# Kernel optimization log

Measured on AMD Instinct MI355X. Metric: run time of the kernel, lower is better.

Reference implementation:

```python
import jax, jax.numpy as jnp
import numpy as np
import math

D_MODEL = 1024
N = 64
TAU_MIN = 1e-4

def _next_pow_two(n: int) -> int:
    return 1 << (n - 1).bit_length()

def setup_inputs() -> dict:
    key = jax.random.key(0)
    ks = jax.random.split(key, 6)
    Bb, T = 4, 8192
    half = N // 2
    n = jnp.arange(half, dtype=jnp.float32)
    x = jax.random.normal(ks[0], (Bb, T, D_MODEL), dtype=jnp.float32)
    log_tau = jnp.full((half,), math.log(0.5), dtype=jnp.float32)
    freq = (math.pi * (2 * n + 1) / 2).astype(jnp.float32)  # hippoD init
    Bp = 1.0 + 0.2 * jax.random.normal(ks[1], (half,), dtype=jnp.float32)
    Cp = (1.0 / math.sqrt(half)) * jax.random.normal(ks[2], (half,), dtype=jnp.float32)
    log_dt = jnp.zeros((), dtype=jnp.float32)
    # torch Linear weight layout: (out_features, in_features)
    W_in = jax.random.normal(ks[3], (half, D_MODEL), dtype=jnp.float32) / math.sqrt(D_MODEL)
    W_out = jax.random.normal(ks[4], (D_MODEL, half), dtype=jnp.float32) / math.sqrt(half)
    return {"x": x, "log_tau": log_tau, "freq": freq, "Bp": Bp, "Cp": Cp,
            "log_dt": log_dt, "W_in": W_in, "W_out": W_out}

def reference(x, log_tau, freq, Bp, Cp, log_dt, W_in, W_out):
    Bb, T, _ = x.shape
    L = _next_pow_two(2 * T)  # static
    half = log_tau.shape[0]
    # ---- analytic kernel (N, T) ----
    dt = jnp.exp(log_dt)
    tau = jnp.clip(jnp.exp(log_tau), TAU_MIN)
    angle = freq * dt                       # (half,)
    log_lam_mag = -tau * dt                 # log of exp(-tau*dt)
    log_gain = jnp.log(jnp.abs(Bp) + 1e-9) + jnp.log(jnp.abs(Cp) + 1e-9)
    i = jnp.arange(T, dtype=x.dtype)
    amp = jnp.exp(log_gain[:, None] + i[None, :] * log_lam_mag[:, None])  # (half, T)
    K_half = amp * jnp.cos(i[None, :] * angle[:, None])                   # (half, T)
    K_full = jnp.concatenate([K_half, K_half[::-1]], axis=0)              # (N, T)
    Kf = jnp.fft.rfft(K_full, n=L, axis=-1)                               # (N, L//2+1)
    # ---- FFT convolution ----
    x_proj = jnp.einsum('btd,nd->btn', x, W_in)                           # (B,T,half)
    x_modes = jnp.concatenate([x_proj, x_proj[..., ::-1]], axis=-1)       # (B,T,N)
    Uf = jnp.fft.rfft(x_modes, n=L, axis=1).transpose(0, 2, 1)            # (B,N,L//2+1)
    Yf = Uf * Kf[None]
    y_modes = jnp.fft.irfft(Yf, n=L, axis=2)[..., :T].transpose(0, 2, 1)  # (B,T,N)
    y = y_modes[..., :half]                                               # (B,T,half)
    return jnp.einsum('btn,dn->btd', y, W_out)
```

## Files before the change

kernel.cpp:

```cpp
#include <hip/hip_runtime.h>
#include <math.h>

#define NB 4
#define TT 8192
#define DM 1024
#define NH 32
#define CT 64
#define NG (TT/CT)
#define DK 128

__global__ __launch_bounds__(256) void k1_proj_scan(
    const float* __restrict__ x, const float* __restrict__ Wi,
    const float* __restrict__ log_tau, const float* __restrict__ freq,
    const float* __restrict__ log_dt,
    float* __restrict__ hl, float* __restrict__ Ech)
{
    __shared__ __align__(16) float xs[CT * 129];
    __shared__ __align__(16) float ws[NH * DK];
    const int c    = blockIdx.x;
    const int b    = blockIdx.y;
    const int t0   = c * CT;
    const int tid  = threadIdx.x;
    const int lane = tid & 63;
    const int ng   = tid >> 6;

    float acc[8] = {0.f, 0.f, 0.f, 0.f, 0.f, 0.f, 0.f, 0.f};
    const float* xb = x + ((size_t)b * TT + t0) * DM;

    for (int dk = 0; dk < DM; dk += DK) {
#pragma unroll
        for (int it = 0; it < 8; ++it) {
            int idx4 = tid + it * 256;
            int tt   = idx4 >> 5;
            int d4   = (idx4 & 31) * 4;
            float4 v = *(const float4*)(xb + (size_t)tt * DM + dk + d4);
            float* p = &xs[tt * 129 + d4];
            p[0] = v.x; p[1] = v.y; p[2] = v.z; p[3] = v.w;
        }
#pragma unroll
        for (int it = 0; it < 4; ++it) {
            int idx4 = tid + it * 256;
            int nn   = idx4 >> 5;
            int d4   = (idx4 & 31) * 4;
            *(float4*)(&ws[nn * DK + d4]) =
                *(const float4*)(Wi + (size_t)nn * DM + dk + d4);
        }
        __syncthreads();
#pragma unroll 2
        for (int d4 = 0; d4 < DK; d4 += 4) {
            const float* xrow = &xs[lane * 129 + d4];
            float x0 = xrow[0], x1 = xrow[1], x2 = xrow[2], x3 = xrow[3];
#pragma unroll
            for (int j = 0; j < 8; ++j) {
                const float4 w = *(const float4*)(&ws[(ng * 8 + j) * DK + d4]);
                acc[j] = fmaf(x3, w.w, fmaf(x2, w.z, fmaf(x1, w.y, fmaf(x0, w.x, acc[j]))));
            }
        }
        __syncthreads();
    }

    const float dtv = expf(log_dt[0]);
    for (int j = 0; j < 8; ++j) {
        const int n = ng * 8 + j;
        const float tau = fmaxf(expf(log_tau[n]), 1e-4f);
        const float rr  = expf(-tau * dtv);
        const float th  = freq[n] * dtv;
        float pr = rr * cosf(th), pi = rr * sinf(th);
        float vr = acc[j], vi = 0.f;
#pragma unroll
        for (int off = 1; off < 64; off <<= 1) {
            float ur = __shfl_up(vr, (unsigned)off);
            float ui = __shfl_up(vi, (unsigned)off);
            if (lane >= off) {
                vr = fmaf(pr, ur, fmaf(-pi, ui, vr));
                vi = fmaf(pr, ui, fmaf( pi, ur, vi));
            }
            float sr = pr * pr - pi * pi;
            float si = 2.f * pr * pi;
            pr = sr; pi = si;
        }
        size_t hb = (((size_t)b * TT + t0 + lane) * NH + n) * 2;
        hl[hb]     = vr;
        hl[hb + 1] = vi;
        if (lane == 63) {
            size_t eb = (((size_t)b * NG + c) * NH + n) * 2;
            Ech[eb]     = vr;
            Ech[eb + 1] = vi;
        }
    }
}

__global__ __launch_bounds__(64) void k2_chunkscan(
    const float* __restrict__ log_tau, const float* __restrict__ freq,
    const float* __restrict__ log_dt,
    const float* __restrict__ Ech, float* __restrict__ Hin)
{
    const int n = threadIdx.x;
    if (n >= NH) return;
    const int c = blockIdx.x;
    const int b = blockIdx.y;
    const double dtv = exp((double)log_dt[0]);
    const double tau = fmax(exp((double)log_tau[n]), 1e-4);
    const double th  = (double)freq[n] * dtv;
    const double m   = exp(-tau * dtv * (double)CT);
    const double a   = th * (double)CT;
    const float Lr = (float)(m * cos(a));
    const float Li = (float)(m * sin(a));
    float hr = 0.f, hi = 0.f;
    for (int cp = 0; cp < c; ++cp) {
        const float* e = Ech + (((size_t)b * NG + cp) * NH + n) * 2;
        float tr = Lr * hr - Li * hi + e[0];
        float ti = Lr * hi + Li * hr + e[1];
        hr = tr; hi = ti;
    }
    float* o = Hin + (((size_t)b * NG + c) * NH + n) * 2;
    o[0] = hr; o[1] = hi;
}

#define ROWFMA(i, s) \
    acc[i].x = fmaf(s, w.x, acc[i].x); acc[i].y = fmaf(s, w.y, acc[i].y); \
    acc[i].z = fmaf(s, w.z, acc[i].z); acc[i].w = fmaf(s, w.w, acc[i].w);

__global__ __launch_bounds__(256) void k3_out(
    const float* __restrict__ hl, const float* __restrict__ Hin,
    const float* __restrict__ Wo,
    const float* __restrict__ log_tau, const float* __restrict__ freq,
    const float* __restrict__ Bp, const float* __restrict__ Cp,
    const float* __restrict__ log_dt,
    float* __restrict__ out)
{
    __shared__ __align__(16) float ysT[NH * 64];
    __shared__ __align__(16) float wT[NH * 260];
    const int c    = blockIdx.x;
    const int b    = blockIdx.y;
    const int t0   = c * CT;
    const int tid  = threadIdx.x;
    const int lane = tid & 63;
    const int ng   = tid >> 6;

    {
        const float dtv = expf(log_dt[0]);
        const int t = lane;
        for (int j = 0; j < 8; ++j) {
            const int n = ng * 8 + j;
            const float tau = fmaxf(expf(log_tau[n]), 1e-4f);
            const float rr  = expf(-tau * dtv);
            const float th  = freq[n] * dtv;
            const float g   = (fabsf(Bp[n]) + 1e-9f) * (fabsf(Cp[n]) + 1e-9f);
            float p2r = rr * cosf(th), p2i = rr * sinf(th);
            float pwr = 1.f, pwi = 0.f;
            const int e = t + 1;
#pragma unroll
            for (int bit = 0; bit < 7; ++bit) {
                if (e & (1 << bit)) {
                    float nr = pwr * p2r - pwi * p2i;
                    float ni = pwr * p2i + pwi * p2r;
                    pwr = nr; pwi = ni;
                }
                float sr = p2r * p2r - p2i * p2i;
                float si = 2.f * p2r * p2i;
                p2r = sr; p2i = si;
            }
            const float* hp = hl  + (((size_t)b * TT + t0 + t) * NH + n) * 2;
            const float* Hp = Hin + (((size_t)b * NG + c) * NH + n) * 2;
            float re = hp[0] + pwr * Hp[0] - pwi * Hp[1];
            ysT[n * 64 + t] = g * re;
        }
    }
    __syncthreads();

    float* const outb = out + ((size_t)b * TT + t0) * DM;
    for (int db = 0; db < DM; db += 256) {
#pragma unroll
        for (int it = 0; it < 32; ++it) {
            int idx = tid + it * 256;
            int dl  = idx >> 5;
            int nn  = idx & 31;
            wT[nn * 260 + dl] = Wo[(size_t)(db + dl) * NH + nn];
        }
        __syncthreads();
        float4 acc[16];
#pragma unroll
        for (int i = 0; i < 16; ++i) acc[i] = make_float4(0.f, 0.f, 0.f, 0.f);
#pragma unroll 4
        for (int n = 0; n < NH; ++n) {
            const float4 w = *(const float4*)(&wT[n * 260 + lane * 4]);
            const float4* yp = (const float4*)(&ysT[n * 64 + ng * 16]);
            const float4 ya = yp[0], yb = yp[1], yc = yp[2], yd = yp[3];
            ROWFMA(0,  ya.x) ROWFMA(1,  ya.y) ROWFMA(2,  ya.z) ROWFMA(3,  ya.w)
            ROWFMA(4,  yb.x) ROWFMA(5,  yb.y) ROWFMA(6,  yb.z) ROWFMA(7,  yb.w)
            ROWFMA(8,  yc.x) ROWFMA(9,  yc.y) ROWFMA(10, yc.z) ROWFMA(11, yc.w)
            ROWFMA(12, yd.x) ROWFMA(13, yd.y) ROWFMA(14, yd.z) ROWFMA(15, yd.w)
        }
#pragma unroll
        for (int i = 0; i < 16; ++i) {
            *(float4*)(outb + (size_t)(ng * 16 + i) * DM + db + lane * 4) = acc[i];
        }
        __syncthreads();
    }
}

extern "C" void kernel_launch(void* const* d_in, const int* in_sizes, int n_in,
                              void* d_out, int out_size, void* d_ws, size_t ws_size,
                              hipStream_t stream)
{
    (void)in_sizes; (void)n_in; (void)out_size; (void)ws_size;
    const float* x       = (const float*)d_in[0];
    const float* log_tau = (const float*)d_in[1];
    const float* freq    = (const float*)d_in[2];
    const float* Bp      = (const float*)d_in[3];
    const float* Cp      = (const float*)d_in[4];
    const float* log_dt  = (const float*)d_in[5];
    const float* Wi      = (const float*)d_in[6];
    const float* Wo      = (const float*)d_in[7];
    float* out = (float*)d_out;

    float* wsf = (float*)d_ws;
    float* hl  = wsf;
    float* Ech = wsf + (size_t)NB * TT * NH * 2;
    float* Hin = Ech + (size_t)NB * NG * NH * 2;

    dim3 grid(NG, NB);
    k1_proj_scan<<<grid, 256, 0, stream>>>(x, Wi, log_tau, freq, log_dt, hl, Ech);
    k2_chunkscan<<<grid, 64, 0, stream>>>(log_tau, freq, log_dt, Ech, Hin);
    k3_out<<<grid, 256, 0, stream>>>(hl, Hin, Wo, log_tau, freq, Bp, Cp, log_dt, out);
}
```

Baseline: 342.5 us.

## Double block size, parallel-scan chunk carries, reorganize hl layout and output tiling

All three kernels are reworked. k1 and k3 move to 512-thread blocks with fewer modes per wave, and k1's shared-memory stores are staggered to cut bank conflicts. k2 replaces the O(NG) sequential carry loop per block with one block per batch that runs a wave-level parallel complex scan over chunk pairs. The intermediate buffers move to a float2 mode-major layout so loads and stores coalesce. k3 tiles its output over 512 columns with scalar strided weight reads, which changes register pressure and the store pattern.

```diff
diff --git a/kernel.cpp b/kernel.cpp
--- a/kernel.cpp
+++ b/kernel.cpp
@@ -8,51 +8,55 @@
 #define CT 64
 #define NG (TT/CT)
 #define DK 128
-
-__global__ __launch_bounds__(256) void k1_proj_scan(
+#define MW 4
+
+__global__ __launch_bounds__(512, 4) void k1_proj_scan(
     const float* __restrict__ x, const float* __restrict__ Wi,
     const float* __restrict__ log_tau, const float* __restrict__ freq,
     const float* __restrict__ log_dt,
-    float* __restrict__ hl, float* __restrict__ Ech)
-{
-    __shared__ __align__(16) float xs[CT * 129];
-    __shared__ __align__(16) float ws[NH * DK];
+    float2* __restrict__ hl, float2* __restrict__ Ech)
+{
+    __shared__ float xs[CT * 129];
+    __shared__ float ws[NH * DK];
     const int c    = blockIdx.x;
     const int b    = blockIdx.y;
     const int t0   = c * CT;
     const int tid  = threadIdx.x;
     const int lane = tid & 63;
-    const int ng   = tid >> 6;
-
-    float acc[8] = {0.f, 0.f, 0.f, 0.f, 0.f, 0.f, 0.f, 0.f};
+    const int wv   = tid >> 6;
+
+    float acc[MW] = {0.f, 0.f, 0.f, 0.f};
     const float* xb = x + ((size_t)b * TT + t0) * DM;
 
     for (int dk = 0; dk < DM; dk += DK) {
 #pragma unroll
-        for (int it = 0; it < 8; ++it) {
-            int idx4 = tid + it * 256;
+        for (int it = 0; it < 4; ++it) {
+            int idx4 = tid + it * 512;
             int tt   = idx4 >> 5;
-            int d4   = (idx4 & 31) * 4;
-            float4 v = *(const float4*)(xb + (size_t)tt * DM + dk + d4);
-            float* p = &xs[tt * 129 + d4];
-            p[0] = v.x; p[1] = v.y; p[2] = v.z; p[3] = v.w;
-        }
-#pragma unroll
-        for (int it = 0; it < 4; ++it) {
-            int idx4 = tid + it * 256;
+            int cc   = idx4 & 31;
+            float4 v = *(const float4*)(xb + (size_t)tt * DM + dk + cc * 4);
+            float vv[4] = {v.x, v.y, v.z, v.w};
+            float* p = &xs[tt * 129 + cc * 4];
+            int q = (idx4 >> 3) & 3;
+#pragma unroll
+            for (int k = 0; k < 4; ++k) { int j = (k + q) & 3; p[j] = vv[j]; }
+        }
+#pragma unroll
+        for (int it = 0; it < 2; ++it) {
+            int idx4 = tid + it * 512;
             int nn   = idx4 >> 5;
             int d4   = (idx4 & 31) * 4;
             *(float4*)(&ws[nn * DK + d4]) =
                 *(const float4*)(Wi + (size_t)nn * DM + dk + d4);
         }
         __syncthreads();
-#pragma unroll 2
+#pragma unroll 4
         for (int d4 = 0; d4 < DK; d4 += 4) {
-            const float* xrow = &xs[lane * 129 + d4];
-            float x0 = xrow[0], x1 = xrow[1], x2 = xrow[2], x3 = xrow[3];
-#pragma unroll
-            for (int j = 0; j < 8; ++j) {
-                const float4 w = *(const float4*)(&ws[(ng * 8 + j) * DK + d4]);
+            const float* xr = &xs[lane * 129 + d4];
+            float x0 = xr[0], x1 = xr[1], x2 = xr[2], x3 = xr[3];
+#pragma unroll
+            for (int j = 0; j < MW; ++j) {
+                const float4 w = *(const float4*)(&ws[(wv * MW + j) * DK + d4]);
                 acc[j] = fmaf(x3, w.w, fmaf(x2, w.z, fmaf(x1, w.y, fmaf(x0, w.x, acc[j]))));
             }
         }
@@ -60,8 +64,9 @@
     }
 
     const float dtv = expf(log_dt[0]);
-    for (int j = 0; j < 8; ++j) {
-        const int n = ng * 8 + j;
+#pragma unroll
+    for (int j = 0; j < MW; ++j) {
+        const int n = wv * MW + j;
         const float tau = fmaxf(expf(log_tau[n]), 1e-4f);
         const float rr  = expf(-tau * dtv);
         const float th  = freq[n] * dtv;
@@ -79,70 +84,81 @@
             float si = 2.f * pr * pi;
             pr = sr; pi = si;
         }
-        size_t hb = (((size_t)b * TT + t0 + lane) * NH + n) * 2;
-        hl[hb]     = vr;
-        hl[hb + 1] = vi;
+        hl[((size_t)(b * NG + c) * NH + n) * CT + lane] = make_float2(vr, vi);
         if (lane == 63) {
-            size_t eb = (((size_t)b * NG + c) * NH + n) * 2;
-            Ech[eb]     = vr;
-            Ech[eb + 1] = vi;
-        }
-    }
-}
-
-__global__ __launch_bounds__(64) void k2_chunkscan(
+            Ech[((size_t)b * NH + n) * NG + c] = make_float2(vr, vi);
+        }
+    }
+}
+
+__global__ __launch_bounds__(256) void k2_chunkscan(
     const float* __restrict__ log_tau, const float* __restrict__ freq,
     const float* __restrict__ log_dt,
-    const float* __restrict__ Ech, float* __restrict__ Hin)
-{
-    const int n = threadIdx.x;
-    if (n >= NH) return;
-    const int c = blockIdx.x;
-    const int b = blockIdx.y;
+    const float2* __restrict__ Ech, float2* __restrict__ Hin)
+{
+    const int b    = blockIdx.x;
+    const int lane = threadIdx.x & 63;
+    const int wv   = threadIdx.x >> 6;
     const double dtv = exp((double)log_dt[0]);
-    const double tau = fmax(exp((double)log_tau[n]), 1e-4);
-    const double th  = (double)freq[n] * dtv;
-    const double m   = exp(-tau * dtv * (double)CT);
-    const double a   = th * (double)CT;
-    const float Lr = (float)(m * cos(a));
-    const float Li = (float)(m * sin(a));
-    float hr = 0.f, hi = 0.f;
-    for (int cp = 0; cp < c; ++cp) {
-        const float* e = Ech + (((size_t)b * NG + cp) * NH + n) * 2;
-        float tr = Lr * hr - Li * hi + e[0];
-        float ti = Lr * hi + Li * hr + e[1];
-        hr = tr; hi = ti;
-    }
-    float* o = Hin + (((size_t)b * NG + c) * NH + n) * 2;
-    o[0] = hr; o[1] = hi;
-}
-
-#define ROWFMA(i, s) \
-    acc[i].x = fmaf(s, w.x, acc[i].x); acc[i].y = fmaf(s, w.y, acc[i].y); \
-    acc[i].z = fmaf(s, w.z, acc[i].z); acc[i].w = fmaf(s, w.w, acc[i].w);
-
-__global__ __launch_bounds__(256) void k3_out(
-    const float* __restrict__ hl, const float* __restrict__ Hin,
+#pragma unroll
+    for (int j = 0; j < 8; ++j) {
+        const int n = wv * 8 + j;
+        const double tau = fmax(exp((double)log_tau[n]), 1e-4);
+        const double a   = (double)freq[n] * dtv * (double)CT;
+        const double m   = exp(-tau * dtv * (double)CT);
+        const float Lr = (float)(m * cos(a));
+        const float Li = (float)(m * sin(a));
+        const float2* eb = Ech + ((size_t)b * NH + n) * NG;
+        float2 e0 = eb[2 * lane];
+        float2 e1 = eb[2 * lane + 1];
+        float vr = fmaf(Lr, e0.x, fmaf(-Li, e0.y, e1.x));
+        float vi = fmaf(Lr, e0.y, fmaf( Li, e0.x, e1.y));
+        float pr = Lr * Lr - Li * Li;
+        float pi = 2.f * Lr * Li;
+#pragma unroll
+        for (int off = 1; off < 64; off <<= 1) {
+            float ur = __shfl_up(vr, (unsigned)off);
+            float ui = __shfl_up(vi, (unsigned)off);
+            if (lane >= off) {
+                vr = fmaf(pr, ur, fmaf(-pi, ui, vr));
+                vi = fmaf(pr, ui, fmaf( pi, ur, vi));
+            }
+            float sr = pr * pr - pi * pi;
+            float si = 2.f * pr * pi;
+            pr = sr; pi = si;
+        }
+        float wr = __shfl_up(vr, 1u), wi = __shfl_up(vi, 1u);
+        if (lane == 0) { wr = 0.f; wi = 0.f; }
+        float2* hb = Hin + ((size_t)b * NH + n) * NG;
+        hb[2 * lane]     = make_float2(wr, wi);
+        hb[2 * lane + 1] = make_float2(fmaf(Lr, wr, fmaf(-Li, wi, e0.x)),
+                                       fmaf(Lr, wi, fmaf( Li, wr, e0.y)));
+    }
+}
+
+__global__ __launch_bounds__(512, 4) void k3_out(
+    const float2* __restrict__ hl, const float2* __restrict__ Hin,
     const float* __restrict__ Wo,
     const float* __restrict__ log_tau, const float* __restrict__ freq,
     const float* __restrict__ Bp, const float* __restrict__ Cp,
     const float* __restrict__ log_dt,
     float* __restrict__ out)
 {
-    __shared__ __align__(16) float ysT[NH * 64];
-    __shared__ __align__(16) float wT[NH * 260];
+    __shared__ float ysT[NH * 64];
+    __shared__ float wT[NH * 513];
     const int c    = blockIdx.x;
     const int b    = blockIdx.y;
     const int t0   = c * CT;
     const int tid  = threadIdx.x;
     const int lane = tid & 63;
-    const int ng   = tid >> 6;
+    const int wv   = tid >> 6;
 
     {
         const float dtv = expf(log_dt[0]);
         const int t = lane;
-        for (int j = 0; j < 8; ++j) {
-            const int n = ng * 8 + j;
+#pragma unroll
+        for (int j = 0; j < 4; ++j) {
+            const int n = wv * 4 + j;
             const float tau = fmaxf(expf(log_tau[n]), 1e-4f);
             const float rr  = expf(-tau * dtv);
             const float th  = freq[n] * dtv;
@@ -161,42 +177,53 @@
                 float si = 2.f * p2r * p2i;
                 p2r = sr; p2i = si;
             }
-            const float* hp = hl  + (((size_t)b * TT + t0 + t) * NH + n) * 2;
-            const float* Hp = Hin + (((size_t)b * NG + c) * NH + n) * 2;
-            float re = hp[0] + pwr * Hp[0] - pwi * Hp[1];
-            ysT[n * 64 + t] = g * re;
-        }
-    }
-    __syncthreads();
-
+            float2 hv = hl[((size_t)(b * NG + c) * NH + n) * CT + t];
+            float2 Hv = Hin[((size_t)b * NH + n) * NG + c];
+            ysT[n * 64 + t] = g * (hv.x + pwr * Hv.x - pwi * Hv.y);
+        }
+    }
+
+    const int qd = wv >> 2;
+    const int tg = wv & 3;
+    const int dbase = qd * 256 + lane;
     float* const outb = out + ((size_t)b * TT + t0) * DM;
-    for (int db = 0; db < DM; db += 256) {
+    for (int db = 0; db < DM; db += 512) {
+        __syncthreads();
 #pragma unroll
         for (int it = 0; it < 32; ++it) {
-            int idx = tid + it * 256;
+            int idx = tid + it * 512;
             int dl  = idx >> 5;
             int nn  = idx & 31;
-            wT[nn * 260 + dl] = Wo[(size_t)(db + dl) * NH + nn];
-        }
-        __syncthreads();
-        float4 acc[16];
-#pragma unroll
-        for (int i = 0; i < 16; ++i) acc[i] = make_float4(0.f, 0.f, 0.f, 0.f);
+            wT[nn * 513 + dl] = Wo[(size_t)(db + dl) * NH + nn];
+        }
+        __syncthreads();
+        float a0[16], a1[16], a2[16], a3[16];
+#pragma unroll
+        for (int i = 0; i < 16; ++i) { a0[i] = a1[i] = a2[i] = a3[i] = 0.f; }
 #pragma unroll 4
         for (int n = 0; n < NH; ++n) {
-            const float4 w = *(const float4*)(&wT[n * 260 + lane * 4]);
-            const float4* yp = (const float4*)(&ysT[n * 64 + ng * 16]);
-            const float4 ya = yp[0], yb = yp[1], yc = yp[2], yd = yp[3];
-            ROWFMA(0,  ya.x) ROWFMA(1,  ya.y) ROWFMA(2,  ya.z) ROWFMA(3,  ya.w)
-            ROWFMA(4,  yb.x) ROWFMA(5,  yb.y) ROWFMA(6,  yb.z) ROWFMA(7,  yb.w)
-            ROWFMA(8,  yc.x) ROWFMA(9,  yc.y) ROWFMA(10, yc.z) ROWFMA(11, yc.w)
-            ROWFMA(12, yd.x) ROWFMA(13, yd.y) ROWFMA(14, yd.z) ROWFMA(15, yd.w)
+            const float w0 = wT[n * 513 + dbase];
+            const float w1 = wT[n * 513 + dbase + 64];
+            const float w2 = wT[n * 513 + dbase + 128];
+            const float w3 = wT[n * 513 + dbase + 192];
+            const float* yr = &ysT[n * 64 + tg * 16];
+#pragma unroll
+            for (int i = 0; i < 16; ++i) {
+                const float yv = yr[i];
+                a0[i] = fmaf(yv, w0, a0[i]);
+                a1[i] = fmaf(yv, w1, a1[i]);
+                a2[i] = fmaf(yv, w2, a2[i]);
+                a3[i] = fmaf(yv, w3, a3[i]);
+            }
         }
 #pragma unroll
         for (int i = 0; i < 16; ++i) {
-            *(float4*)(outb + (size_t)(ng * 16 + i) * DM + db + lane * 4) = acc[i];
-        }
-        __syncthreads();
+            float* op = outb + (size_t)(tg * 16 + i) * DM + db + dbase;
+            op[0]   = a0[i];
+            op[64]  = a1[i];
+            op[128] = a2[i];
+            op[192] = a3[i];
+        }
     }
 }
 
@@ -215,13 +242,12 @@
     const float* Wo      = (const float*)d_in[7];
     float* out = (float*)d_out;
 
-    float* wsf = (float*)d_ws;
-    float* hl  = wsf;
-    float* Ech = wsf + (size_t)NB * TT * NH * 2;
-    float* Hin = Ech + (size_t)NB * NG * NH * 2;
+    float2* hl  = (float2*)d_ws;
+    float2* Ech = hl  + (size_t)NB * NG * NH * CT;
+    float2* Hin = Ech + (size_t)NB * NH * NG;
 
     dim3 grid(NG, NB);
-    k1_proj_scan<<<grid, 256, 0, stream>>>(x, Wi, log_tau, freq, log_dt, hl, Ech);
-    k2_chunkscan<<<grid, 64, 0, stream>>>(log_tau, freq, log_dt, Ech, Hin);
-    k3_out<<<grid, 256, 0, stream>>>(hl, Hin, Wo, log_tau, freq, Bp, Cp, log_dt, out);
-}
+    k1_proj_scan<<<grid, 512, 0, stream>>>(x, Wi, log_tau, freq, log_dt, hl, Ech);
+    k2_chunkscan<<<NB, 256, 0, stream>>>(log_tau, freq, log_dt, Ech, Hin);
+    k3_out<<<grid, 512, 0, stream>>>(hl, Hin, Wo, log_tau, freq, Bp, Cp, log_dt, out);
+}
```

After: 320.1 us. 1.07x faster.
